# Optimization experiments

Measured on AMD Instinct MI355X. Metric: run time of the kernel, lower is better.

The kernel has to match this reference:

```python
import jax, jax.numpy as jnp
import numpy as np

TEMPERATURE = 0.1
LOSS_SCALE = 1.0
LAMBD = 0.5


def setup_inputs() -> dict:
    key = jax.random.key(0)
    k1, k2 = jax.random.split(key)
    B, D = 4096, 768
    predicted = jax.random.normal(k1, (B, D), dtype=jnp.float32)
    target = jax.random.normal(k2, (B, D), dtype=jnp.float32)
    return {"predicted": predicted, "target": target}


def reference(predicted, target):
    predicted = predicted.astype(jnp.float32)
    target = target.astype(jnp.float32)
    B = predicted.shape[0]

    # Pairwise L2 distances via Gram identity (avoids B x B x D intermediate):
    # ||p_i - t_j||^2 = ||p_i||^2 + ||t_j||^2 - 2 p_i . t_j
    p_sq = jnp.sum(predicted * predicted, axis=-1)  # [B]
    t_sq = jnp.sum(target * target, axis=-1)        # [B]
    cross = predicted @ target.T                    # [B, B]
    sq_dist = p_sq[:, None] + t_sq[None, :] - 2.0 * cross
    distances = jnp.sqrt(jnp.maximum(sq_dist, 0.0))  # [B, B]

    logits = -distances / TEMPERATURE
    # cross-entropy with labels = arange(B): mean of -log_softmax diagonal
    log_probs = jax.nn.log_softmax(logits, axis=-1)
    contrastive_dist_loss = -jnp.mean(jnp.diagonal(log_probs))

    # normalized L1 magnitude loss
    elementwise_l1 = jnp.sum(jnp.abs(predicted - target), axis=-1)  # [B]
    target_magnitude = jnp.sum(jnp.abs(target), axis=-1)            # [B]
    norm_factor = jax.lax.stop_gradient(target_magnitude)
    normalized_magnitude_loss = jnp.mean(elementwise_l1 / norm_factor)

    total_loss = LOSS_SCALE * (
        LAMBD * contrastive_dist_loss + (1.0 - LAMBD) * normalized_magnitude_loss
    )
    return (total_loss, contrastive_dist_loss, normalized_magnitude_loss)
```

## Files before the change

### kernel.cpp

```cpp
#include <hip/hip_runtime.h>
#include <hip/hip_bf16.h>
#include <math.h>

#define B_ROWS 4096
#define D_DIM  768

#define BM 128
#define BN 128
#define BK 64

typedef __attribute__((ext_vector_type(8))) short bf16x8;
typedef __attribute__((ext_vector_type(4))) float f32x4;

__device__ __forceinline__ unsigned short f32_to_bf16(float x) {
    unsigned int u = __float_as_uint(x);
    return (unsigned short)((u + 0x7fffu + ((u >> 16) & 1u)) >> 16);
}

__device__ __forceinline__ void async_copy16(const unsigned short* g, unsigned short* l) {
    __builtin_amdgcn_global_load_lds(
        (const __attribute__((address_space(1))) unsigned int*)g,
        (__attribute__((address_space(3))) unsigned int*)l,
        16, 0, 0);
}

__global__ void __launch_bounds__(256) rowstats_kernel(
    const float* __restrict__ P, const float* __restrict__ T,
    unsigned short* __restrict__ Pb, unsigned short* __restrict__ Tb,
    float* __restrict__ p_sq, float* __restrict__ t_sq,
    float* __restrict__ diagl, float* __restrict__ magr,
    float* __restrict__ rowsum)
{
    const int wave = threadIdx.x >> 6, lane = threadIdx.x & 63;
    const int i = blockIdx.x * 4 + wave;
    const f32x4* prow = (const f32x4*)(P + (size_t)i * D_DIM);
    const f32x4* trow = (const f32x4*)(T + (size_t)i * D_DIM);
    ushort4* pbrow = (ushort4*)(Pb + (size_t)i * D_DIM);
    ushort4* tbrow = (ushort4*)(Tb + (size_t)i * D_DIM);

    float psq = 0.f, tsq = 0.f, cr = 0.f, l1 = 0.f, tm = 0.f;
    #pragma unroll
    for (int u = 0; u < 3; ++u) {
        const int c4 = u * 64 + lane;
        f32x4 p = prow[c4], t = trow[c4];
        #pragma unroll
        for (int k = 0; k < 4; ++k) {
            psq += p[k] * p[k]; tsq += t[k] * t[k]; cr += p[k] * t[k];
            l1 += fabsf(p[k] - t[k]); tm += fabsf(t[k]);
        }
        pbrow[c4] = make_ushort4(f32_to_bf16(p[0]), f32_to_bf16(p[1]),
                                 f32_to_bf16(p[2]), f32_to_bf16(p[3]));
        tbrow[c4] = make_ushort4(f32_to_bf16(t[0]), f32_to_bf16(t[1]),
                                 f32_to_bf16(t[2]), f32_to_bf16(t[3]));
    }
    #pragma unroll
    for (int m = 1; m < 64; m <<= 1) {
        psq += __shfl_xor(psq, m, 64);
        tsq += __shfl_xor(tsq, m, 64);
        cr  += __shfl_xor(cr,  m, 64);
        l1  += __shfl_xor(l1,  m, 64);
        tm  += __shfl_xor(tm,  m, 64);
    }
    if (lane == 0) {
        p_sq[i] = psq;
        t_sq[i] = tsq;
        float sq = fmaxf(psq + tsq - 2.0f * cr, 0.0f);
        diagl[i] = -sqrtf(sq) * 10.0f;
        magr[i]  = l1 / tm;
        rowsum[i] = 0.0f;
    }
}

__global__ void __launch_bounds__(256) lse_gemm_kernel(
    const unsigned short* __restrict__ Pb, const unsigned short* __restrict__ Tb,
    const float* __restrict__ p_sq, const float* __restrict__ t_sq,
    const float* __restrict__ diagl, float* __restrict__ rowsum)
{
    __shared__ __align__(16) unsigned short As[BM * BK];
    __shared__ __align__(16) unsigned short Bs[BN * BK];

    const int tid = threadIdx.x;
    const int i0 = blockIdx.y * BM;
    const int j0 = blockIdx.x * BN;

    const int lane  = tid & 63;
    const int wave  = tid >> 6;
    const int wm    = wave >> 1, wn = wave & 1;
    const int row16 = lane & 15, quad = lane >> 4;
    const int m_base = wm * 64, n_base = wn * 64;

    const int lrow   = lane >> 3;
    const int lchunk = (lane & 7) ^ lrow;
    const int swz = (quad ^ (row16 & 7)) << 4;

    f32x4 acc[4][4];
    #pragma unroll
    for (int a = 0; a < 4; ++a)
        #pragma unroll
        for (int b = 0; b < 4; ++b)
            acc[a][b] = (f32x4){0.f, 0.f, 0.f, 0.f};

    const char* Ab = (const char*)As;
    const char* Bb = (const char*)Bs;

    for (int kt = 0; kt < D_DIM; kt += BK) {
        #pragma unroll
        for (int it = 0; it < 4; ++it) {
            const int r = wave * 32 + it * 8 + lrow;
            async_copy16(Pb + (size_t)(i0 + r) * D_DIM + kt + lchunk * 8,
                         &As[(wave * 4 + it) * 512]);
        }
        #pragma unroll
        for (int it = 0; it < 4; ++it) {
            const int r = wave * 32 + it * 8 + lrow;
            async_copy16(Tb + (size_t)(j0 + r) * D_DIM + kt + lchunk * 8,
                         &Bs[(wave * 4 + it) * 512]);
        }
        __syncthreads();

        #pragma unroll
        for (int ks = 0; ks < BK; ks += 32) {
            const int kx = ks ? 64 : 0;
            bf16x8 a[4], b[4];
            #pragma unroll
            for (int mt = 0; mt < 4; ++mt) {
                const int off = (m_base + mt * 16 + row16) * 128 + swz;
                a[mt] = *(const bf16x8*)(Ab + (off ^ kx));
            }
            #pragma unroll
            for (int nt = 0; nt < 4; ++nt) {
                const int off = (n_base + nt * 16 + row16) * 128 + swz;
                b[nt] = *(const bf16x8*)(Bb + (off ^ kx));
            }
            #pragma unroll
            for (int mt = 0; mt < 4; ++mt)
                #pragma unroll
                for (int nt = 0; nt < 4; ++nt)
                    acc[mt][nt] = __builtin_amdgcn_mfma_f32_16x16x32_bf16(
                        a[mt], b[nt], acc[mt][nt], 0, 0, 0);
        }
        __syncthreads();
    }

    const float NT_LOG2E = -14.4269504089f;
    const float LOG2E    = 1.44269504089f;
    float tsq_l[4];
    #pragma unroll
    for (int nt = 0; nt < 4; ++nt)
        tsq_l[nt] = t_sq[j0 + n_base + nt * 16 + row16];

    #pragma unroll
    for (int mt = 0; mt < 4; ++mt) {
        #pragma unroll
        for (int r = 0; r < 4; ++r) {
            const int i = i0 + m_base + mt * 16 + quad * 4 + r;
            const float psq = p_sq[i];
            const float c0  = -diagl[i] * LOG2E;
            float s = 0.f;
            #pragma unroll
            for (int nt = 0; nt < 4; ++nt) {
                float c  = acc[mt][nt][r];
                float sq = fmaxf(fmaf(-2.0f, c, psq + tsq_l[nt]), 0.0f);
                float d  = sqrtf(sq);
                float y  = fmaf(d, NT_LOG2E, c0);
                s += exp2f(y);
            }
            #pragma unroll
            for (int m = 1; m < 16; m <<= 1) s += __shfl_xor(s, m, 64);
            if (row16 == 0) atomicAdd(&rowsum[i], s);
        }
    }
}

__global__ void __launch_bounds__(256) finalize_kernel(
    const float* __restrict__ rowsum, const float* __restrict__ magr,
    float* __restrict__ out)
{
    const int tid = threadIdx.x;
    double sc = 0.0, sm = 0.0;
    for (int i = tid; i < B_ROWS; i += 256) {
        sc += log((double)rowsum[i]);
        sm += (double)magr[i];
    }
    #pragma unroll
    for (int m = 1; m < 64; m <<= 1) {
        sc += __shfl_xor(sc, m, 64);
        sm += __shfl_xor(sm, m, 64);
    }
    __shared__ double red[4][2];
    const int wave = tid >> 6, lane = tid & 63;
    if (lane == 0) { red[wave][0] = sc; red[wave][1] = sm; }
    __syncthreads();
    if (tid == 0) {
        sc = red[0][0] + red[1][0] + red[2][0] + red[3][0];
        sm = red[0][1] + red[1][1] + red[2][1] + red[3][1];
        double lc = sc / (double)B_ROWS;
        double lm = sm / (double)B_ROWS;
        out[0] = (float)(0.5 * lc + 0.5 * lm);
        out[1] = (float)lc;
        out[2] = (float)lm;
    }
}

extern "C" void kernel_launch(void* const* d_in, const int* in_sizes, int n_in,
                              void* d_out, int out_size, void* d_ws, size_t ws_size,
                              hipStream_t stream) {
    const float* P = (const float*)d_in[0];
    const float* T = (const float*)d_in[1];
    float* out = (float*)d_out;

    char* ws = (char*)d_ws;
    float* rowsum = (float*)ws;               ws += B_ROWS * sizeof(float);
    float* p_sq   = (float*)ws;               ws += B_ROWS * sizeof(float);
    float* t_sq   = (float*)ws;               ws += B_ROWS * sizeof(float);
    float* diagl  = (float*)ws;               ws += B_ROWS * sizeof(float);
    float* magr   = (float*)ws;               ws += B_ROWS * sizeof(float);
    unsigned short* Pb = (unsigned short*)ws; ws += (size_t)B_ROWS * D_DIM * 2;
    unsigned short* Tb = (unsigned short*)ws;

    rowstats_kernel<<<B_ROWS / 4, 256, 0, stream>>>(
        P, T, Pb, Tb, p_sq, t_sq, diagl, magr, rowsum);
    lse_gemm_kernel<<<dim3(B_ROWS / BN, B_ROWS / BM), 256, 0, stream>>>(
        Pb, Tb, p_sq, t_sq, diagl, rowsum);
    finalize_kernel<<<1, 256, 0, stream>>>(rowsum, magr, out);
}
```

Measured before the change: 133.7 us.

## Double-buffer LDS tiles and remap blocks for XCD-aware L2 locality

```diff
diff --git a/kernel.cpp b/kernel.cpp
--- a/kernel.cpp
+++ b/kernel.cpp
@@ -8,6 +8,7 @@
 #define BM 128
 #define BN 128
 #define BK 64
+#define NKT (D_DIM / BK)
 
 typedef __attribute__((ext_vector_type(8))) short bf16x8;
 typedef __attribute__((ext_vector_type(4))) float f32x4;
@@ -76,12 +77,18 @@
     const float* __restrict__ p_sq, const float* __restrict__ t_sq,
     const float* __restrict__ diagl, float* __restrict__ rowsum)
 {
-    __shared__ __align__(16) unsigned short As[BM * BK];
-    __shared__ __align__(16) unsigned short Bs[BN * BK];
+    __shared__ __align__(16) unsigned short As[2][BM * BK];
+    __shared__ __align__(16) unsigned short Bs[2][BN * BK];
 
     const int tid = threadIdx.x;
-    const int i0 = blockIdx.y * BM;
-    const int j0 = blockIdx.x * BN;
+
+    const int flat = blockIdx.y * (B_ROWS / BN) + blockIdx.x;
+    const int xcd  = flat & 7;
+    const int s    = flat >> 3;
+    const int g    = xcd + ((s >> 6) << 3);
+    const int w    = s & 63;
+    const int i0   = (((g >> 2) << 3) + (w >> 3)) * BM;
+    const int j0   = (((g & 3) << 3) + (w & 7)) * BN;
 
     const int lane  = tid & 63;
     const int wave  = tid >> 6;
@@ -93,6 +100,15 @@
     const int lchunk = (lane & 7) ^ lrow;
     const int swz = (quad ^ (row16 & 7)) << 4;
 
+    const unsigned short* pg[4];
+    const unsigned short* tg[4];
+    #pragma unroll
+    for (int it = 0; it < 4; ++it) {
+        const int r = wave * 32 + it * 8 + lrow;
+        pg[it] = Pb + (size_t)(i0 + r) * D_DIM + lchunk * 8;
+        tg[it] = Tb + (size_t)(j0 + r) * D_DIM + lchunk * 8;
+    }
+
     f32x4 acc[4][4];
     #pragma unroll
     for (int a = 0; a < 4; ++a)
@@ -100,24 +116,27 @@
         for (int b = 0; b < 4; ++b)
             acc[a][b] = (f32x4){0.f, 0.f, 0.f, 0.f};
 
-    const char* Ab = (const char*)As;
-    const char* Bb = (const char*)Bs;
-
-    for (int kt = 0; kt < D_DIM; kt += BK) {
-        #pragma unroll
-        for (int it = 0; it < 4; ++it) {
-            const int r = wave * 32 + it * 8 + lrow;
-            async_copy16(Pb + (size_t)(i0 + r) * D_DIM + kt + lchunk * 8,
-                         &As[(wave * 4 + it) * 512]);
-        }
-        #pragma unroll
-        for (int it = 0; it < 4; ++it) {
-            const int r = wave * 32 + it * 8 + lrow;
-            async_copy16(Tb + (size_t)(j0 + r) * D_DIM + kt + lchunk * 8,
-                         &Bs[(wave * 4 + it) * 512]);
-        }
+    #pragma unroll
+    for (int it = 0; it < 4; ++it) {
+        async_copy16(pg[it], &As[0][(wave * 4 + it) * 512]);
+        async_copy16(tg[it], &Bs[0][(wave * 4 + it) * 512]);
+    }
+
+    for (int ktile = 0; ktile < NKT; ++ktile) {
+        const int sel = ktile & 1;
         __syncthreads();
 
+        if (ktile + 1 < NKT) {
+            const int kt1 = (ktile + 1) * BK;
+            #pragma unroll
+            for (int it = 0; it < 4; ++it) {
+                async_copy16(pg[it] + kt1, &As[sel ^ 1][(wave * 4 + it) * 512]);
+                async_copy16(tg[it] + kt1, &Bs[sel ^ 1][(wave * 4 + it) * 512]);
+            }
+        }
+
+        const char* Ab = (const char*)As[sel];
+        const char* Bb = (const char*)Bs[sel];
         #pragma unroll
         for (int ks = 0; ks < BK; ks += 32) {
             const int kx = ks ? 64 : 0;
@@ -139,7 +158,6 @@
                     acc[mt][nt] = __builtin_amdgcn_mfma_f32_16x16x32_bf16(
                         a[mt], b[nt], acc[mt][nt], 0, 0, 0);
         }
-        __syncthreads();
     }
 
     const float NT_LOG2E = -14.4269504089f;
@@ -156,18 +174,18 @@
             const int i = i0 + m_base + mt * 16 + quad * 4 + r;
             const float psq = p_sq[i];
             const float c0  = -diagl[i] * LOG2E;
-            float s = 0.f;
+            float sfin = 0.f;
             #pragma unroll
             for (int nt = 0; nt < 4; ++nt) {
                 float c  = acc[mt][nt][r];
                 float sq = fmaxf(fmaf(-2.0f, c, psq + tsq_l[nt]), 0.0f);
                 float d  = sqrtf(sq);
                 float y  = fmaf(d, NT_LOG2E, c0);
-                s += exp2f(y);
-            }
-            #pragma unroll
-            for (int m = 1; m < 16; m <<= 1) s += __shfl_xor(s, m, 64);
-            if (row16 == 0) atomicAdd(&rowsum[i], s);
+                sfin += exp2f(y);
+            }
+            #pragma unroll
+            for (int m = 1; m < 16; m <<= 1) sfin += __shfl_xor(sfin, m, 64);
+            if (row16 == 0) atomicAdd(&rowsum[i], sfin);
         }
     }
 }
```

New measurement: 131.2 us. Within noise of the previous version (-1.9%).
